# Kernel optimization log

Hardware: AMD Instinct MI355X
Metric: run time of the kernel (lower is better)

## Reference

```python
import jax, jax.numpy as jnp
import numpy as np

D_MODEL = 1024
N_HEADS = 16
D_HEAD = D_MODEL // N_HEADS
D_FF = 4096
B, T = 2, 2048
EPS = 1e-6


def setup_inputs() -> dict:
    key = jax.random.key(0)
    ks = jax.random.split(key, 10)
    s = 0.02
    return {
        "x": jax.random.normal(ks[0], (B, T, D_MODEL), dtype=jnp.float32),
        # Linear weights stored as (in, out) so y = x @ W (equivalent to torch x @ W.T)
        "Wq": jax.random.normal(ks[1], (D_MODEL, D_MODEL), dtype=jnp.float32) * s,
        "Wk": jax.random.normal(ks[2], (D_MODEL, D_MODEL), dtype=jnp.float32) * s,
        "Wv": jax.random.normal(ks[3], (D_MODEL, D_MODEL), dtype=jnp.float32) * s,
        "Wo": jax.random.normal(ks[4], (D_MODEL, D_MODEL), dtype=jnp.float32) * s,
        "W1": jax.random.normal(ks[5], (D_MODEL, D_FF), dtype=jnp.float32) * s,
        "b1": jnp.zeros((D_FF,), dtype=jnp.float32),
        "W2": jax.random.normal(ks[6], (D_FF, D_MODEL), dtype=jnp.float32) * s,
        "b2": jnp.zeros((D_MODEL,), dtype=jnp.float32),
        "g1": jnp.ones((D_MODEL,), dtype=jnp.float32),
        "g2": jnp.ones((D_MODEL,), dtype=jnp.float32),
    }


def rmsnorm(x, g):
    return x * jax.lax.rsqrt(jnp.mean(x * x, axis=-1, keepdims=True) + EPS) * g


def attention(x, Wq, Wk, Wv, Wo):
    b, t, c = x.shape
    def split_heads(y):  # [B,T,C] -> [B,H,T,Dh]
        return y.reshape(b, t, N_HEADS, D_HEAD).transpose(0, 2, 1, 3)
    q = split_heads(x @ Wq)
    k = split_heads(x @ Wk)
    v = split_heads(x @ Wv)
    att = jnp.einsum("bhqd,bhkd->bhqk", q, k) / jnp.sqrt(jnp.float32(D_HEAD))
    causal = jnp.tril(jnp.ones((t, t), dtype=bool))
    att = jnp.where(causal[None, None], att, -jnp.inf)
    att = jax.nn.softmax(att, axis=-1)
    y = jnp.einsum("bhqk,bhkd->bhqd", att, v)
    y = y.transpose(0, 2, 1, 3).reshape(b, t, c)
    return y @ Wo


def reference(x, Wq, Wk, Wv, Wo, W1, b1, W2, b2, g1, g2):
    x = x + attention(rmsnorm(x, g1), Wq, Wk, Wv, Wo)
    h = rmsnorm(x, g2)
    h = jax.nn.gelu(h @ W1 + b1, approximate=False) @ W2 + b2
    return x + h
```

## Files before the change

### kernel.cpp

```cpp
#include <hip/hip_runtime.h>
#include <hip/hip_bf16.h>
#include <math.h>
#include <stdint.h>


typedef __bf16 v8bf  __attribute__((ext_vector_type(8)));
typedef float  v4f   __attribute__((ext_vector_type(4)));

#define T_SEQ 2048
#define EXP2F(x) __builtin_amdgcn_exp2f(x)

#define FRAG(base, R, ko) \
  (*(const v8bf*)((base) + (R) * 64 + (((((ko) >> 3) ^ ((R) & 7))) << 3)))

__device__ __forceinline__ void async_ld16(const void* g, void* l) {
  __builtin_amdgcn_global_load_lds(
      (const __attribute__((address_space(1))) uint32_t*)g,
      (__attribute__((address_space(3))) uint32_t*)l, 16, 0, 0);
}

__device__ __forceinline__ void wg_barrier() {
  asm volatile("" ::: "memory");
  __builtin_amdgcn_s_barrier();
  asm volatile("" ::: "memory");
}

__global__ __launch_bounds__(256) void transpose_w4(
    const float* __restrict__ Wq, const float* __restrict__ Wk,
    const float* __restrict__ Wv, const float* __restrict__ Wo,
    __hip_bfloat16* __restrict__ out)
{
  __shared__ float tile[32][33];
  const int z = blockIdx.z;
  const float* W = z == 0 ? Wq : z == 1 ? Wk : z == 2 ? Wv : Wo;
  const int n0 = blockIdx.x * 32, k0 = blockIdx.y * 32;
  const int tx = threadIdx.x, ty = threadIdx.y;
#pragma unroll
  for (int i = 0; i < 32; i += 8)
    tile[ty + i][tx] = W[(size_t)(k0 + ty + i) * 1024 + n0 + tx];
  __syncthreads();
  __hip_bfloat16* o = out + (size_t)z * 1024 * 1024;
#pragma unroll
  for (int i = 0; i < 32; i += 8)
    o[(size_t)(n0 + ty + i) * 1024 + k0 + tx] = __float2bfloat16(tile[tx][ty + i]);
}

__global__ __launch_bounds__(256) void transpose_w(
    const float* __restrict__ W, __hip_bfloat16* __restrict__ WT,
    int K, int N, int ldo)
{
  __shared__ float tile[32][33];
  const int n0 = blockIdx.x * 32, k0 = blockIdx.y * 32;
  const int tx = threadIdx.x, ty = threadIdx.y;
#pragma unroll
  for (int i = 0; i < 32; i += 8)
    tile[ty + i][tx] = W[(size_t)(k0 + ty + i) * N + n0 + tx];
  __syncthreads();
#pragma unroll
  for (int i = 0; i < 32; i += 8)
    WT[(size_t)(n0 + ty + i) * ldo + k0 + tx] = __float2bfloat16(tile[tx][ty + i]);
}

__global__ __launch_bounds__(256) void transpose_v(
    const __hip_bfloat16* __restrict__ QKV, __hip_bfloat16* __restrict__ VTg)
{
  __shared__ float tile[32][33];
  const int t0 = blockIdx.x * 32;
  const int bh = blockIdx.y >> 1;
  const int dt = (blockIdx.y & 1) * 32;
  const int b = bh >> 4, h = bh & 15;
  const int tx = threadIdx.x, ty = threadIdx.y;
#pragma unroll
  for (int i = 0; i < 32; i += 8)
    tile[ty + i][tx] = __bfloat162float(
        QKV[(size_t)(b * T_SEQ + t0 + ty + i) * 3072 + 2048 + h * 64 + dt + tx]);
  __syncthreads();
#pragma unroll
  for (int i = 0; i < 32; i += 8)
    VTg[((size_t)bh * 64 + dt + ty + i) * T_SEQ + t0 + tx] =
        __float2bfloat16(tile[tx][ty + i]);
}

__global__ __launch_bounds__(256) void rmsnorm_kernel(
    const float* __restrict__ x, const float* __restrict__ g,
    __hip_bfloat16* __restrict__ out,
    const float* __restrict__ bias, float* __restrict__ dinit)
{
  const int row = blockIdx.x;
  const int t = threadIdx.x;
  const float4 v = ((const float4*)(x + (size_t)row * 1024))[t];
  float ss = v.x * v.x + v.y * v.y + v.z * v.z + v.w * v.w;
#pragma unroll
  for (int off = 32; off; off >>= 1) ss += __shfl_xor(ss, off, 64);
  __shared__ float red[4];
  if ((t & 63) == 0) red[t >> 6] = ss;
  __syncthreads();
  ss = red[0] + red[1] + red[2] + red[3];
  const float rs = rsqrtf(ss * (1.0f / 1024.0f) + 1e-6f);
  const float4 gv = ((const float4*)g)[t];
  __hip_bfloat16* o = out + (size_t)row * 1024 + t * 4;
  o[0] = __float2bfloat16(v.x * rs * gv.x);
  o[1] = __float2bfloat16(v.y * rs * gv.y);
  o[2] = __float2bfloat16(v.z * rs * gv.z);
  o[3] = __float2bfloat16(v.w * rs * gv.w);
  if (dinit) {
    const float4 bv = ((const float4*)bias)[t];
    float4 d;
    d.x = v.x + bv.x; d.y = v.y + bv.y; d.z = v.z + bv.z; d.w = v.w + bv.w;
    ((float4*)(dinit + (size_t)row * 1024))[t] = d;
  }
}

template <int MODE, int MT, int PX, int PY>
__global__ __launch_bounds__(256, 2) void gemm_bt(
    const __hip_bfloat16* __restrict__ A,
    const __hip_bfloat16* __restrict__ BT,
    const float* __restrict__ bias,
    const float* __restrict__ resid,
    __hip_bfloat16* __restrict__ outb,
    float* __restrict__ outf,
    int M, int N, int K, int Ksub)
{
  __shared__ __align__(16) __hip_bfloat16 As[32 * MT * 64];
  __shared__ __align__(16) __hip_bfloat16 Bs[128 * 64];
  const int tid = threadIdx.x;
  const int wave = tid >> 6, lane = tid & 63;
  const int quad = lane >> 4, l16 = lane & 15;

  int bx = blockIdx.x, by = blockIdx.y;
  {
    const int id = by * gridDim.x + bx;
    const int k = id & 7, s = id >> 3;
    const int pw = gridDim.x / PX, ph = gridDim.y / PY;
    bx = (k % PX) * pw + (s % pw);
    by = (k / PX) * ph + (s / pw);
  }
  const int m0 = by * (32 * MT), n0 = bx * 128;
  const size_t kb = (size_t)blockIdx.z * Ksub;
  const int wr = (wave >> 1) * (16 * MT), wc = (wave & 1) * 64;
  const int lrow = lane >> 3;
  const int scol = ((lane & 7) ^ lrow) * 8;

  v4f acc[MT][4];
#pragma unroll
  for (int i = 0; i < MT; i++)
#pragma unroll
    for (int j = 0; j < 4; j++)
#pragma unroll
      for (int c = 0; c < 4; c++) acc[i][j][c] = 0.0f;

  for (int k0 = 0; k0 < Ksub; k0 += 64) {
#pragma unroll
    for (int i = 0; i < MT + 4; i++) {
      const int c = wave * (MT + 4) + i;
      if (c < 4 * MT) {
        async_ld16(A + (size_t)(m0 + c * 8 + lrow) * K + kb + k0 + scol, As + c * 512);
      } else {
        const int cb = c - 4 * MT;
        async_ld16(BT + (size_t)(n0 + cb * 8 + lrow) * K + kb + k0 + scol,
                   Bs + cb * 512);
      }
    }
    __syncthreads();
#pragma unroll
    for (int ks = 0; ks < 64; ks += 32) {
      v8bf af[MT], bfr[4];
#pragma unroll
      for (int mt = 0; mt < MT; mt++)
        af[mt] = FRAG(As, wr + mt * 16 + l16, ks + quad * 8);
#pragma unroll
      for (int nt = 0; nt < 4; nt++)
        bfr[nt] = FRAG(Bs, wc + nt * 16 + l16, ks + quad * 8);
#pragma unroll
      for (int mt = 0; mt < MT; mt++)
#pragma unroll
        for (int nt = 0; nt < 4; nt++)
          acc[mt][nt] = __builtin_amdgcn_mfma_f32_16x16x32_bf16(
              af[mt], bfr[nt], acc[mt][nt], 0, 0, 0);
    }
    __syncthreads();
  }

#pragma unroll
  for (int mt = 0; mt < MT; mt++) {
#pragma unroll
    for (int r = 0; r < 4; r++) {
      const int gm = m0 + wr + mt * 16 + quad * 4 + r;
#pragma unroll
      for (int nt = 0; nt < 4; nt++) {
        const int gn = n0 + wc + nt * 16 + l16;
        float v = acc[mt][nt][r];
        if (MODE == 0) {
          outb[(size_t)gm * N + gn] = __float2bfloat16(v);
        } else if (MODE == 1) {
          outf[(size_t)gm * N + gn] = resid[(size_t)gm * N + gn] + v;
        } else if (MODE == 2) {
          v += bias[gn];
          const float u = 0.7978845608f * (v + 0.044715f * v * v * v);
          const float e = EXP2F(u * 2.885390082f);
          const float th = 1.0f - 2.0f * __builtin_amdgcn_rcpf(e + 1.0f);
          v = 0.5f * v * (1.0f + th);
          outb[(size_t)gm * N + gn] = __float2bfloat16(v);
        } else {
          atomicAdd(&outf[(size_t)gm * N + gn], v);
        }
      }
    }
  }
}

template <int MODE, int PX, int PY>
__global__ __launch_bounds__(512, 2) void gemm256(
    const __hip_bfloat16* __restrict__ A,
    const __hip_bfloat16* __restrict__ BT,
    const float* __restrict__ bias,
    __hip_bfloat16* __restrict__ outb,
    float* __restrict__ outf,
    int M, int N, int K, int Ksub)
{
  __shared__ __align__(16) __hip_bfloat16 As[2 * 256 * 64];
  __shared__ __align__(16) __hip_bfloat16 Bs[2 * 256 * 64];
  (void)M;
  const int tid = threadIdx.x;
  const int wave = tid >> 6, lane = tid & 63;
  const int quad = lane >> 4, l16 = lane & 15;
  const int wm = wave >> 2, wn = wave & 3;
  const int lrow = lane >> 3, scol = ((lane & 7) ^ lrow) * 8;

  int bx = blockIdx.x, by = blockIdx.y;
  {
    const int id = by * gridDim.x + bx;
    const int k = id & 7, s = id >> 3;
    const int pw = gridDim.x / PX, ph = gridDim.y / PY;
    bx = (k % PX) * pw + (s % pw);
    by = (k / PX) * ph + (s / pw);
  }
  const int m0 = by * 256, n0 = bx * 256;
  const size_t kb = (size_t)blockIdx.z * Ksub;
  const int NT = Ksub >> 6;
  const int cg = wave * 2;

  auto stageA = [&](int h, int tt) {
#pragma unroll
    for (int j = 0; j < 2; j++) {
      const int rg = cg + j;
      async_ld16(A + (size_t)(m0 + h * 128 + rg * 8 + lrow) * K + kb + tt * 64 + scol,
                 As + ((tt & 1) * 16384 + (h * 128 + rg * 8) * 64));
    }
  };
  auto stageB = [&](int h, int tt) {
#pragma unroll
    for (int j = 0; j < 2; j++) {
      const int rg = cg + j;
      async_ld16(BT + (size_t)(n0 + h * 128 + rg * 8 + lrow) * K + kb + tt * 64 + scol,
                 Bs + ((tt & 1) * 16384 + (h * 128 + rg * 8) * 64));
    }
  };

  v4f acc[8][4];
#pragma unroll
  for (int i = 0; i < 8; i++)
#pragma unroll
    for (int j = 0; j < 4; j++)
#pragma unroll
      for (int c = 0; c < 4; c++) acc[i][j][c] = 0.0f;

  stageA(0, 0); stageB(0, 0); stageB(1, 0); stageA(1, 0);
  if (NT > 1) {
    stageA(0, 1); stageB(1, 1);
    asm volatile("s_waitcnt vmcnt(4)" ::: "memory");
  } else {
    asm volatile("s_waitcnt vmcnt(0)" ::: "memory");
  }
  wg_barrier();

#define READ_A(mh)                                                          \
  _Pragma("unroll") for (int mt = 0; mt < 4; mt++)                          \
      _Pragma("unroll") for (int ks = 0; ks < 2; ks++)                      \
          af[mt][ks] =                                                      \
              FRAG(Ab, (mh) * 128 + wm * 64 + mt * 16 + l16, ks * 32 + quad * 8)
#define READ_B(dst, nh)                                                     \
  _Pragma("unroll") for (int nt = 0; nt < 2; nt++)                          \
      _Pragma("unroll") for (int ks = 0; ks < 2; ks++)                      \
          dst[nt][ks] =                                                     \
              FRAG(Bb, (nh) * 128 + wn * 32 + nt * 16 + l16, ks * 32 + quad * 8)
#define MM16(mh, bsrc, nh)                                                  \
  __builtin_amdgcn_s_setprio(1);                                            \
  _Pragma("unroll") for (int mt = 0; mt < 4; mt++)                          \
      _Pragma("unroll") for (int nt = 0; nt < 2; nt++)                      \
          _Pragma("unroll") for (int ks = 0; ks < 2; ks++)                  \
              acc[(mh) * 4 + mt][(nh) * 2 + nt] =                           \
                  __builtin_amdgcn_mfma_f32_16x16x32_bf16(                  \
                      af[mt][ks], bsrc[nt][ks],                             \
                      acc[(mh) * 4 + mt][(nh) * 2 + nt], 0, 0, 0);          \
  __builtin_amdgcn_s_setprio(0)

  for (int t = 0; t < NT; ++t) {
    const __hip_bfloat16* Ab = As + (t & 1) * 16384;
    const __hip_bfloat16* Bb = Bs + (t & 1) * 16384;
    v8bf af[4][2], b0[2][2], b1[2][2];
    READ_A(0); READ_B(b0, 0);
    if (t + 1 < NT) stageA(1, t + 1);
    wg_barrier();
    MM16(0, b0, 0);
    wg_barrier();
    READ_B(b1, 1);
    if (t + 1 < NT) stageB(0, t + 1);
    wg_barrier();
    MM16(0, b1, 1);
    wg_barrier();
    READ_A(1);
    if (t + 2 < NT) stageA(0, t + 2);
    wg_barrier();
    MM16(1, b1, 1);
    wg_barrier();
    if (t + 2 < NT) stageB(1, t + 2);
    wg_barrier();
    MM16(1, b0, 0);
    if (t + 2 < NT) {
      asm volatile("s_waitcnt vmcnt(4)" ::: "memory");
    } else if (t + 1 < NT) {
      asm volatile("s_waitcnt vmcnt(0)" ::: "memory");
    }
    wg_barrier();
  }
#undef READ_A
#undef READ_B
#undef MM16

#pragma unroll
  for (int ni = 0; ni < 4; ni++) {
    const int gn = n0 + (ni >> 1) * 128 + wn * 32 + (ni & 1) * 16 + l16;
    float bcol = 0.0f;
    if (MODE == 2) bcol = bias[gn];
#pragma unroll
    for (int mi = 0; mi < 8; mi++) {
      const int gmb = m0 + (mi >> 2) * 128 + wm * 64 + (mi & 3) * 16 + quad * 4;
#pragma unroll
      for (int r = 0; r < 4; r++) {
        float v = acc[mi][ni][r];
        const size_t idx = (size_t)(gmb + r) * N + gn;
        if (MODE == 0) {
          outb[idx] = __float2bfloat16(v);
        } else if (MODE == 2) {
          v += bcol;
          const float u = 0.7978845608f * (v + 0.044715f * v * v * v);
          const float e = EXP2F(u * 2.885390082f);
          const float th = 1.0f - 2.0f * __builtin_amdgcn_rcpf(e + 1.0f);
          v = 0.5f * v * (1.0f + th);
          outb[idx] = __float2bfloat16(v);
        } else {
          atomicAdd(&outf[idx], v);
        }
      }
    }
  }
}

__global__ __launch_bounds__(256, 2) void attn_kernel(
    const __hip_bfloat16* __restrict__ QKV,
    const __hip_bfloat16* __restrict__ VTg,
    __hip_bfloat16* __restrict__ Y)
{
  __shared__ __align__(16) __hip_bfloat16 Ks[2 * 64 * 64];
  __shared__ __align__(16) __hip_bfloat16 Vs[2 * 64 * 64];
  __shared__ __align__(16) __hip_bfloat16 PsA[64 * 64];
  __shared__ __align__(16) __hip_bfloat16 PsB[64 * 64];

  const int tid = threadIdx.x;
  const int wave = tid >> 6, lane = tid & 63;
  const int quad = lane >> 4, l16 = lane & 15;
  const int blk = blockIdx.x;
  const int p = blk & 15, h = (blk >> 4) & 15, b = blk >> 8;
  const int qa = p, qb = 31 - p, kmax = qb;
  const size_t rowbase = (size_t)b * T_SEQ;
  const size_t vbase = (size_t)(b * 16 + h) * 64;
  const int lrow = lane >> 3, scol = ((lane & 7) ^ (lane >> 3)) * 8;

  const float QSC = 0.125f * 1.44269504f;
  v8bf aqA[2], aqB[2];
#pragma unroll
  for (int ks = 0; ks < 2; ks++) {
    v8bf q = *(const v8bf*)(QKV + (rowbase + qa * 64 + wave * 16 + l16) * 3072 +
                            h * 64 + ks * 32 + quad * 8);
#pragma unroll
    for (int j = 0; j < 8; j++) aqA[ks][j] = (__bf16)((float)q[j] * QSC);
    q = *(const v8bf*)(QKV + (rowbase + qb * 64 + wave * 16 + l16) * 3072 +
                       h * 64 + ks * 32 + quad * 8);
#pragma unroll
    for (int j = 0; j < 8; j++) aqB[ks][j] = (__bf16)((float)q[j] * QSC);
  }

  v4f oA[4], oB[4];
  float lpA[4], lpB[4];
#pragma unroll
  for (int i = 0; i < 4; i++) {
    lpA[i] = 0.0f; lpB[i] = 0.0f;
#pragma unroll
    for (int c = 0; c < 4; c++) { oA[i][c] = 0.0f; oB[i][c] = 0.0f; }
  }

  auto stage = [&](int kt, int buf) {
#pragma unroll
    for (int i = 0; i < 2; i++) {
      const int r8 = i * 32 + wave * 8;
      const int rr = r8 + lrow;
      async_ld16(QKV + (rowbase + kt * 64 + rr) * 3072 + 1024 + h * 64 + scol,
                 Ks + buf * 4096 + r8 * 64);
      async_ld16(VTg + (vbase + rr) * T_SEQ + kt * 64 + scol,
                 Vs + buf * 4096 + r8 * 64);
    }
  };
  stage(0, 0);

  auto softmax_store = [&](v4f s[4], float lp[4], __hip_bfloat16* Ps, bool diag) {
    if (diag) {
#pragma unroll
      for (int nt = 0; nt < 4; nt++) {
        const int colr = nt * 16 + l16;
#pragma unroll
        for (int r = 0; r < 4; r++)
          if (colr > wave * 16 + quad * 4 + r) s[nt][r] = -30000.0f;
      }
    }
#pragma unroll
    for (int r = 0; r < 4; r++) {
      const int row = wave * 16 + quad * 4 + r;
      const int rsw = (quad * 4 + r) & 7;
#pragma unroll
      for (int nt = 0; nt < 4; nt++) {
        const float e = EXP2F(s[nt][r]);
        lp[r] += e;
        const int chunk = (nt * 2 + (l16 >> 3)) ^ rsw;
        Ps[row * 64 + (chunk << 3) + (l16 & 7)] = __float2bfloat16(e);
      }
    }
  };

  for (int kt = 0; kt <= kmax; kt++) {
    __syncthreads();
    if (kt < kmax) stage(kt + 1, (kt + 1) & 1);
    const __hip_bfloat16* Kb = Ks + (kt & 1) * 4096;
    const __hip_bfloat16* Vb = Vs + (kt & 1) * 4096;
    const bool doA = (kt <= qa);

    {
      v8bf kf[2][4];
#pragma unroll
      for (int ks = 0; ks < 2; ks++)
#pragma unroll
        for (int nt = 0; nt < 4; nt++)
          kf[ks][nt] = FRAG(Kb, nt * 16 + l16, ks * 32 + quad * 8);

      v4f sB[4];
#pragma unroll
      for (int nt = 0; nt < 4; nt++)
#pragma unroll
        for (int c = 0; c < 4; c++) sB[nt][c] = 0.0f;
#pragma unroll
      for (int ks = 0; ks < 2; ks++)
#pragma unroll
        for (int nt = 0; nt < 4; nt++)
          sB[nt] = __builtin_amdgcn_mfma_f32_16x16x32_bf16(aqB[ks], kf[ks][nt],
                                                           sB[nt], 0, 0, 0);
      softmax_store(sB, lpB, PsB, kt == qb);

      if (doA) {
        v4f sA[4];
#pragma unroll
        for (int nt = 0; nt < 4; nt++)
#pragma unroll
          for (int c = 0; c < 4; c++) sA[nt][c] = 0.0f;
#pragma unroll
        for (int ks = 0; ks < 2; ks++)
#pragma unroll
          for (int nt = 0; nt < 4; nt++)
            sA[nt] = __builtin_amdgcn_mfma_f32_16x16x32_bf16(aqA[ks], kf[ks][nt],
                                                             sA[nt], 0, 0, 0);
        softmax_store(sA, lpA, PsA, kt == qa);
      }
    }

    {
      v8bf vf[2][4];
#pragma unroll
      for (int ks = 0; ks < 2; ks++)
#pragma unroll
        for (int nt = 0; nt < 4; nt++)
          vf[ks][nt] = FRAG(Vb, nt * 16 + l16, ks * 32 + quad * 8);
#pragma unroll
      for (int ks = 0; ks < 2; ks++) {
        const v8bf apB = FRAG(PsB, wave * 16 + l16, ks * 32 + quad * 8);
#pragma unroll
        for (int nt = 0; nt < 4; nt++)
          oB[nt] = __builtin_amdgcn_mfma_f32_16x16x32_bf16(apB, vf[ks][nt],
                                                           oB[nt], 0, 0, 0);
      }
      if (doA) {
#pragma unroll
        for (int ks = 0; ks < 2; ks++) {
          const v8bf apA = FRAG(PsA, wave * 16 + l16, ks * 32 + quad * 8);
#pragma unroll
          for (int nt = 0; nt < 4; nt++)
            oA[nt] = __builtin_amdgcn_mfma_f32_16x16x32_bf16(apA, vf[ks][nt],
                                                             oA[nt], 0, 0, 0);
        }
      }
    }
  }

#pragma unroll
  for (int r = 0; r < 4; r++) {
    float la = lpA[r], lb = lpB[r];
#pragma unroll
    for (int off = 1; off < 16; off <<= 1) {
      la += __shfl_xor(la, off, 16);
      lb += __shfl_xor(lb, off, 16);
    }
    const float ila = 1.0f / la, ilb = 1.0f / lb;
#pragma unroll
    for (int nt = 0; nt < 4; nt++) {
      Y[(rowbase + qa * 64 + wave * 16 + quad * 4 + r) * 1024 + h * 64 + nt * 16 + l16] =
          __float2bfloat16(oA[nt][r] * ila);
      Y[(rowbase + qb * 64 + wave * 16 + quad * 4 + r) * 1024 + h * 64 + nt * 16 + l16] =
          __float2bfloat16(oB[nt][r] * ilb);
    }
  }
}

extern "C" void kernel_launch(void* const* d_in, const int* in_sizes, int n_in,
                              void* d_out, int out_size, void* d_ws, size_t ws_size,
                              hipStream_t stream)
{
  const float* x  = (const float*)d_in[0];
  const float* Wq = (const float*)d_in[1];
  const float* Wk = (const float*)d_in[2];
  const float* Wv = (const float*)d_in[3];
  const float* Wo = (const float*)d_in[4];
  const float* W1 = (const float*)d_in[5];
  const float* b1 = (const float*)d_in[6];
  const float* W2 = (const float*)d_in[7];
  const float* b2 = (const float*)d_in[8];
  const float* g1 = (const float*)d_in[9];
  const float* g2 = (const float*)d_in[10];

  uint8_t* ws = (uint8_t*)d_ws;
  __hip_bfloat16* WqkvT = (__hip_bfloat16*)(ws + 0);
  __hip_bfloat16* WoT   = (__hip_bfloat16*)(ws + 6291456);
  __hip_bfloat16* W1T   = (__hip_bfloat16*)(ws + 8388608);
  __hip_bfloat16* W2T   = (__hip_bfloat16*)(ws + 16777216);
  float*          x1    = (float*)(ws + 25165824);
  __hip_bfloat16* xn    = (__hip_bfloat16*)(ws + 41943040);
  __hip_bfloat16* Ybuf  = (__hip_bfloat16*)(ws + 41943040);
  __hip_bfloat16* QKV   = (__hip_bfloat16*)(ws + 50331648);
  __hip_bfloat16* VTg   = (__hip_bfloat16*)(ws + 75497472);
  __hip_bfloat16* Hbuf  = (__hip_bfloat16*)(ws + 50331648);

  const dim3 tb(32, 8);
  transpose_w4<<<dim3(32, 32, 4), tb, 0, stream>>>(Wq, Wk, Wv, Wo, WqkvT);
  transpose_w<<<dim3(128, 32), tb, 0, stream>>>(W1, W1T, 1024, 4096, 1024);
  transpose_w<<<dim3(32, 128), tb, 0, stream>>>(W2, W2T, 4096, 1024, 4096);

  rmsnorm_kernel<<<4096, 256, 0, stream>>>(x, g1, xn, nullptr, nullptr);
  gemm256<0, 4, 2><<<dim3(12, 16), 512, 0, stream>>>(
      xn, WqkvT, nullptr, QKV, nullptr, 4096, 3072, 1024, 1024);
  transpose_v<<<dim3(64, 64), tb, 0, stream>>>(QKV, VTg);
  attn_kernel<<<512, 256, 0, stream>>>(QKV, VTg, Ybuf);
  gemm_bt<1, 2, 1, 8><<<dim3(8, 64), 256, 0, stream>>>(
      Ybuf, WoT, nullptr, x, nullptr, x1, 4096, 1024, 1024, 1024);
  rmsnorm_kernel<<<4096, 256, 0, stream>>>(x1, g2, xn, b2, (float*)d_out);
  gemm256<2, 4, 2><<<dim3(16, 16), 512, 0, stream>>>(
      xn, W1T, b1, Hbuf, nullptr, 4096, 4096, 1024, 1024);
  gemm256<4, 4, 2><<<dim3(4, 16, 4), 512, 0, stream>>>(
      Hbuf, W2T, nullptr, nullptr, (float*)d_out, 4096, 1024, 4096, 1024);
}
```

Measured before the change: 353.0 us.

## Use inline-asm LDS reads with explicit lgkmcnt waits and move W2 GEMM to gemm_bt

Replaces the compiler-generated LDS fragment loads in gemm256 with inline ds_read_b128 using precomputed swizzled LDS addresses. Compiler memory fences are swapped for explicit lgkmcnt waits and sched barriers, so the MFMA/LDS interleaving is controlled by hand. One barrier is dropped before the last MFMA block. The down-projection GEMM moves from gemm256 split-K 4 to gemm_bt with split-K 2, so the atomic-add epilogue is removed from gemm256. This risks races between LDS reads and async stage writes if the removed barrier or fences mattered.

```diff
diff --git a/kernel.cpp b/kernel.cpp
--- a/kernel.cpp
+++ b/kernel.cpp
@@ -19,11 +19,21 @@
       (__attribute__((address_space(3))) uint32_t*)l, 16, 0, 0);
 }
 
-__device__ __forceinline__ void wg_barrier() {
-  asm volatile("" ::: "memory");
-  __builtin_amdgcn_s_barrier();
-  asm volatile("" ::: "memory");
-}
+__device__ __forceinline__ uint32_t lds_addr(const void* p) {
+  return (uint32_t)(uintptr_t)(const __attribute__((address_space(3))) void*)p;
+}
+
+__device__ __forceinline__ v8bf ds_read16(uint32_t a) {
+  v8bf r;
+  asm volatile("ds_read_b128 %0, %1" : "=v"(r) : "v"(a));
+  return r;
+}
+
+#define WAITL                                  \
+  do {                                         \
+    asm volatile("s_waitcnt lgkmcnt(0)");      \
+    __builtin_amdgcn_sched_barrier(0);         \
+  } while (0)
 
 __global__ __launch_bounds__(256) void transpose_w4(
     const float* __restrict__ Wq, const float* __restrict__ Wk,
@@ -220,7 +230,7 @@
 {
   __shared__ __align__(16) __hip_bfloat16 As[2 * 256 * 64];
   __shared__ __align__(16) __hip_bfloat16 Bs[2 * 256 * 64];
-  (void)M;
+  (void)M; (void)outf;
   const int tid = threadIdx.x;
   const int wave = tid >> 6, lane = tid & 63;
   const int quad = lane >> 4, l16 = lane & 15;
@@ -240,6 +250,16 @@
   const int NT = Ksub >> 6;
   const int cg = wave * 2;
 
+  uint32_t AsL = lds_addr(As), BsL = lds_addr(Bs);
+  asm volatile("" : "+s"(AsL), "+s"(BsL));
+
+  const uint32_t cx0 = (uint32_t)(((0 * 4 + quad) ^ (l16 & 7)) * 16);
+  const uint32_t cx1 = (uint32_t)(((1 * 4 + quad) ^ (l16 & 7)) * 16);
+  const uint32_t aB0 = AsL + (uint32_t)((wm * 64 + l16) * 128) + cx0;
+  const uint32_t aB1 = AsL + (uint32_t)((wm * 64 + l16) * 128) + cx1;
+  const uint32_t bB0 = BsL + (uint32_t)((wn * 32 + l16) * 128) + cx0;
+  const uint32_t bB1 = BsL + (uint32_t)((wn * 32 + l16) * 128) + cx1;
+
   auto stageA = [&](int h, int tt) {
 #pragma unroll
     for (int j = 0; j < 2; j++) {
@@ -268,22 +288,22 @@
   stageA(0, 0); stageB(0, 0); stageB(1, 0); stageA(1, 0);
   if (NT > 1) {
     stageA(0, 1); stageB(1, 1);
-    asm volatile("s_waitcnt vmcnt(4)" ::: "memory");
+    asm volatile("s_waitcnt vmcnt(4)");
   } else {
-    asm volatile("s_waitcnt vmcnt(0)" ::: "memory");
-  }
-  wg_barrier();
-
-#define READ_A(mh)                                                          \
-  _Pragma("unroll") for (int mt = 0; mt < 4; mt++)                          \
-      _Pragma("unroll") for (int ks = 0; ks < 2; ks++)                      \
-          af[mt][ks] =                                                      \
-              FRAG(Ab, (mh) * 128 + wm * 64 + mt * 16 + l16, ks * 32 + quad * 8)
-#define READ_B(dst, nh)                                                     \
-  _Pragma("unroll") for (int nt = 0; nt < 2; nt++)                          \
-      _Pragma("unroll") for (int ks = 0; ks < 2; ks++)                      \
-          dst[nt][ks] =                                                     \
-              FRAG(Bb, (nh) * 128 + wn * 32 + nt * 16 + l16, ks * 32 + quad * 8)
+    asm volatile("s_waitcnt vmcnt(0)");
+  }
+  __builtin_amdgcn_s_barrier();
+
+#define RA(mh)                                                      \
+  _Pragma("unroll") for (int mt = 0; mt < 4; mt++) {                \
+    af[mt][0] = ds_read16(a0a + (mh) * 16384 + mt * 2048);          \
+    af[mt][1] = ds_read16(a1a + (mh) * 16384 + mt * 2048);          \
+  }
+#define RB(dst, nh)                                                 \
+  _Pragma("unroll") for (int nt = 0; nt < 2; nt++) {                \
+    dst[nt][0] = ds_read16(b0a + (nh) * 16384 + nt * 2048);         \
+    dst[nt][1] = ds_read16(b1a + (nh) * 16384 + nt * 2048);         \
+  }
 #define MM16(mh, bsrc, nh)                                                  \
   __builtin_amdgcn_s_setprio(1);                                            \
   _Pragma("unroll") for (int mt = 0; mt < 4; mt++)                          \
@@ -296,36 +316,40 @@
   __builtin_amdgcn_s_setprio(0)
 
   for (int t = 0; t < NT; ++t) {
-    const __hip_bfloat16* Ab = As + (t & 1) * 16384;
-    const __hip_bfloat16* Bb = Bs + (t & 1) * 16384;
+    const uint32_t bsel = (uint32_t)((t & 1) * 32768);
+    const uint32_t a0a = aB0 + bsel, a1a = aB1 + bsel;
+    const uint32_t b0a = bB0 + bsel, b1a = bB1 + bsel;
     v8bf af[4][2], b0[2][2], b1[2][2];
-    READ_A(0); READ_B(b0, 0);
+    RA(0); RB(b0, 0);
     if (t + 1 < NT) stageA(1, t + 1);
-    wg_barrier();
+    __builtin_amdgcn_s_barrier();
+    WAITL;
     MM16(0, b0, 0);
-    wg_barrier();
-    READ_B(b1, 1);
+    __builtin_amdgcn_s_barrier();
+    RB(b1, 1);
     if (t + 1 < NT) stageB(0, t + 1);
-    wg_barrier();
+    __builtin_amdgcn_s_barrier();
+    WAITL;
     MM16(0, b1, 1);
-    wg_barrier();
-    READ_A(1);
+    __builtin_amdgcn_s_barrier();
+    RA(1);
     if (t + 2 < NT) stageA(0, t + 2);
-    wg_barrier();
+    __builtin_amdgcn_s_barrier();
+    WAITL;
     MM16(1, b1, 1);
-    wg_barrier();
+    __builtin_amdgcn_s_barrier();
     if (t + 2 < NT) stageB(1, t + 2);
-    wg_barrier();
+    WAITL;
     MM16(1, b0, 0);
     if (t + 2 < NT) {
-      asm volatile("s_waitcnt vmcnt(4)" ::: "memory");
+      asm volatile("s_waitcnt vmcnt(4)");
     } else if (t + 1 < NT) {
-      asm volatile("s_waitcnt vmcnt(0)" ::: "memory");
-    }
-    wg_barrier();
-  }
-#undef READ_A
-#undef READ_B
+      asm volatile("s_waitcnt vmcnt(0)");
+    }
+    __builtin_amdgcn_s_barrier();
+  }
+#undef RA
+#undef RB
 #undef MM16
 
 #pragma unroll
@@ -342,15 +366,13 @@
         const size_t idx = (size_t)(gmb + r) * N + gn;
         if (MODE == 0) {
           outb[idx] = __float2bfloat16(v);
-        } else if (MODE == 2) {
+        } else {
           v += bcol;
           const float u = 0.7978845608f * (v + 0.044715f * v * v * v);
           const float e = EXP2F(u * 2.885390082f);
           const float th = 1.0f - 2.0f * __builtin_amdgcn_rcpf(e + 1.0f);
           v = 0.5f * v * (1.0f + th);
           outb[idx] = __float2bfloat16(v);
-        } else {
-          atomicAdd(&outf[idx], v);
         }
       }
     }
@@ -571,6 +593,6 @@
   rmsnorm_kernel<<<4096, 256, 0, stream>>>(x1, g2, xn, b2, (float*)d_out);
   gemm256<2, 4, 2><<<dim3(16, 16), 512, 0, stream>>>(
       xn, W1T, b1, Hbuf, nullptr, 4096, 4096, 1024, 1024);
-  gemm256<4, 4, 2><<<dim3(4, 16, 4), 512, 0, stream>>>(
-      Hbuf, W2T, nullptr, nullptr, (float*)d_out, 4096, 1024, 4096, 1024);
-}
+  gemm_bt<4, 2, 1, 8><<<dim3(8, 64, 2), 256, 0, stream>>>(
+      Hbuf, W2T, nullptr, nullptr, nullptr, (float*)d_out, 4096, 1024, 4096, 2048);
+}
```

Result: faster. 331.7 us (-6.0%).
